# Performance work log

Measured on AMD Instinct MI355X. Metric: run time of the kernel, lower is better.

Reference implementation:

```python
import math
import jax, jax.numpy as jnp
import numpy as np

B, S, D, H, DH, R, V = 8, 1024, 1024, 8, 512, 36, 32002  # DH = d_model//2, HD = h*DH = 4096
HD = H * DH
LN_EPS = 1e-5


def setup_inputs() -> dict:
    key = jax.random.key(0)
    ks = jax.random.split(key, 16)

    def n(k, shp, std=0.02):
        return jax.random.normal(k, shp, jnp.float32) * std

    pre_words = jax.random.randint(ks[0], (B, S), 0, V)
    img_features = jax.random.normal(ks[1], (B, R, D), jnp.float32)
    exp_embed = n(ks[2], (V, D)).at[0].set(0.0)  # padding_idx=0
    # id2visual table: sparse nonneg rows over 36 regions; zero rows -> textual tokens
    id2vis = (jax.random.uniform(ks[3], (V, R)) < 0.05).astype(jnp.float32)
    # stacked params for 2 transformer layers; weights stored (in, out) so y = x @ W + b
    wq = n(ks[4], (2, D, HD)); bq = jnp.zeros((2, HD), jnp.float32)
    wk = n(ks[5], (2, D, HD)); bk = jnp.zeros((2, HD), jnp.float32)
    wv = n(ks[6], (2, D, HD)); bv = jnp.zeros((2, HD), jnp.float32)
    wo = n(ks[7], (2, HD, D)); bo = jnp.zeros((2, D), jnp.float32)
    w1 = n(ks[8], (2, D, D)); b1 = jnp.zeros((2, D), jnp.float32)
    w2 = n(ks[9], (2, D, D)); b2 = jnp.zeros((2, D), jnp.float32)
    ln1_g = jnp.ones((2, D), jnp.float32); ln1_b = jnp.zeros((2, D), jnp.float32)
    ln2_g = jnp.ones((2, D), jnp.float32); ln2_b = jnp.zeros((2, D), jnp.float32)
    return dict(pre_words=pre_words, img_features=img_features, exp_embed=exp_embed,
                id2vis=id2vis, wq=wq, bq=bq, wk=wk, bk=bk, wv=wv, bv=bv, wo=wo, bo=bo,
                w1=w1, b1=b1, w2=w2, b2=b2, ln1_g=ln1_g, ln1_b=ln1_b, ln2_g=ln2_g, ln2_b=ln2_b)


def _layer_norm(x, g, b):
    m = x.mean(-1, keepdims=True)
    v = ((x - m) ** 2).mean(-1, keepdims=True)
    return (x - m) / jnp.sqrt(v + LN_EPS) * g + b


def _softmax_one(x):
    # shifted-denominator softmax: exp(x - max) / (1 + sum exp(x - max))
    x = x - x.max(-1, keepdims=True)
    e = jnp.exp(x)
    return e / (1.0 + e.sum(-1, keepdims=True))


def reference(pre_words, img_features, exp_embed, id2vis, wq, bq, wk, bk, wv, bv,
              wo, bo, w1, b1, w2, b2, ln1_g, ln1_b, ln2_g, ln2_b):
    # token embedding: textual (masked to 0 where a visual row exists) + visual bmm
    te = exp_embed[pre_words]                       # (B,S,D)
    vids = id2vis[pre_words]                        # (B,S,R)
    word_mask = vids.sum(-1, keepdims=True) != 0    # (B,S,1)
    ve = jnp.einsum('bsr,brd->bsd', vids, img_features)
    x = jnp.where(word_mask, 0.0, te) + ve          # (B,S,D)

    scale = 1.0 / math.sqrt(DH)
    for i in range(2):  # two structurally identical transformer layers
        h = _layer_norm(x, ln1_g[i], ln1_b[i])
        q = (h @ wq[i] + bq[i]).reshape(B, S, H, DH).transpose(0, 2, 1, 3)
        k = (h @ wk[i] + bk[i]).reshape(B, S, H, DH).transpose(0, 2, 1, 3)
        v = (h @ wv[i] + bv[i]).reshape(B, S, H, DH).transpose(0, 2, 1, 3)
        attn = _softmax_one(jnp.einsum('bhqd,bhkd->bhqk', q, k) * scale)  # (B,H,S,S)
        o = jnp.einsum('bhqk,bhkd->bhqd', attn, v)
        o = o.transpose(0, 2, 1, 3).reshape(B, S, HD)
        x = x + (o @ wo[i] + bo[i])
        f = _layer_norm(x, ln2_g[i], ln2_b[i])
        f = jax.nn.gelu(f @ w1[i] + b1[i], approximate=False) @ w2[i] + b2[i]
        x = x + f
    return x
```

## Files before the change

### kernel.cpp

```cpp
#include <hip/hip_runtime.h>


using u16 = unsigned short;
typedef __attribute__((ext_vector_type(8))) short bf16x8;
typedef __attribute__((ext_vector_type(4))) float f32x4;

__device__ __forceinline__ float b2f(u16 u) {
  union { unsigned int i; float f; } v; v.i = ((unsigned int)u) << 16; return v.f;
}
__device__ __forceinline__ u16 f2b(float f) {
  union { float f; unsigned int i; } v; v.f = f;
  unsigned int i = v.i;
  return (u16)((i + 0x7FFFu + ((i >> 16) & 1u)) >> 16);
}
__device__ __forceinline__ float gelu_f(float x) {
  return 0.5f * x * (1.f + erff(x * 0.70710678118654752f));
}
__device__ __forceinline__ void async16(void* lds, const void* g) {
  __builtin_amdgcn_global_load_lds((const __attribute__((address_space(1))) void*)g,
                                   (__attribute__((address_space(3))) void*)lds, 16, 0, 0);
}
__device__ __forceinline__ void storeC(float* p, float v) { *p = v; }
__device__ __forceinline__ void storeC(u16* p, float v) { *p = f2b(v); }

__global__ __launch_bounds__(256) void embed_k(
    const int* __restrict__ words, const float* __restrict__ img,
    const float* __restrict__ emb, const float* __restrict__ id2v,
    float* __restrict__ x)
{
  __shared__ float vs[36];
  int tok = blockIdx.x, b = tok >> 10, t = threadIdx.x;
  int wd = words[tok];
  if (t < 36) vs[t] = id2v[(size_t)wd * 36 + t];
  __syncthreads();
  bool any = false;
#pragma unroll
  for (int r = 0; r < 36; ++r) any = any || (vs[r] != 0.f);
#pragma unroll
  for (int i = 0; i < 4; ++i) {
    int d = t + (i << 8);
    float acc = 0.f;
    for (int r = 0; r < 36; ++r) {
      float vv = vs[r];
      if (vv != 0.f) acc += vv * img[((size_t)(b * 36 + r) << 10) + d];
    }
    float te = any ? 0.f : emb[((size_t)wd << 10) + d];
    x[((size_t)tok << 10) + d] = te + acc;
  }
}

__global__ __launch_bounds__(256) void ln_k(
    const float* __restrict__ x, u16* __restrict__ out,
    const float* __restrict__ g, const float* __restrict__ bb)
{
  __shared__ float red[4];
  int row = blockIdx.x, t = threadIdx.x;
  const float4 xv = *(const float4*)(x + ((size_t)row << 10) + (t << 2));
  float s = xv.x + xv.y + xv.z + xv.w;
#pragma unroll
  for (int o = 32; o; o >>= 1) s += __shfl_xor(s, o, 64);
  if ((t & 63) == 0) red[t >> 6] = s;
  __syncthreads();
  s = red[0] + red[1] + red[2] + red[3];
  float mean = s * 0.0009765625f;
  float dx = xv.x - mean, dy = xv.y - mean, dz = xv.z - mean, dw = xv.w - mean;
  float q = dx * dx + dy * dy + dz * dz + dw * dw;
  __syncthreads();
#pragma unroll
  for (int o = 32; o; o >>= 1) q += __shfl_xor(q, o, 64);
  if ((t & 63) == 0) red[t >> 6] = q;
  __syncthreads();
  q = red[0] + red[1] + red[2] + red[3];
  float rstd = rsqrtf(q * 0.0009765625f + 1e-5f);
  const float4 gv = *(const float4*)(g + (t << 2));
  const float4 bv = *(const float4*)(bb + (t << 2));
  ushort4 o4;
  o4.x = f2b(dx * rstd * gv.x + bv.x);
  o4.y = f2b(dy * rstd * gv.y + bv.y);
  o4.z = f2b(dz * rstd * gv.z + bv.z);
  o4.w = f2b(dw * rstd * gv.w + bv.w);
  *(ushort4*)(out + ((size_t)row << 10) + (t << 2)) = o4;
}

__global__ __launch_bounds__(256) void sm_k(const u16* __restrict__ S, u16* __restrict__ P)
{
  size_t row = ((size_t)blockIdx.x << 2) + (threadIdx.x >> 6);
  const int lane = threadIdx.x & 63;
  const u16* sr = S + (row << 10) + (lane << 4);
  ushort4 sv[4];
#pragma unroll
  for (int i = 0; i < 4; ++i) sv[i] = *(const ushort4*)(sr + (i << 2));
  float v[16];
#pragma unroll
  for (int i = 0; i < 4; ++i) {
    v[4 * i + 0] = b2f(sv[i].x); v[4 * i + 1] = b2f(sv[i].y);
    v[4 * i + 2] = b2f(sv[i].z); v[4 * i + 3] = b2f(sv[i].w);
  }
  float m = v[0];
#pragma unroll
  for (int i = 1; i < 16; ++i) m = fmaxf(m, v[i]);
#pragma unroll
  for (int o = 32; o; o >>= 1) m = fmaxf(m, __shfl_xor(m, o, 64));
  float s = 0.f;
#pragma unroll
  for (int i = 0; i < 16; ++i) { v[i] = __expf(v[i] - m); s += v[i]; }
#pragma unroll
  for (int o = 32; o; o >>= 1) s += __shfl_xor(s, o, 64);
  const float inv = 1.f / (1.f + s);
  u16* pr = P + (row << 10) + (lane << 4);
#pragma unroll
  for (int i = 0; i < 4; ++i) {
    ushort4 pv;
    pv.x = f2b(v[4 * i + 0] * inv); pv.y = f2b(v[4 * i + 1] * inv);
    pv.z = f2b(v[4 * i + 2] * inv); pv.w = f2b(v[4 * i + 3] * inv);
    *(ushort4*)(pr + (i << 2)) = pv;
  }
}

__global__ __launch_bounds__(256) void tr_k(
    const float* __restrict__ src, u16* __restrict__ dst, int ls, int ld)
{
  __shared__ u16 tile[64][65];
  int c0 = blockIdx.x << 6, r0 = blockIdx.y << 6;
  int tx = threadIdx.x & 63, ty0 = threadIdx.x >> 6;
#pragma unroll
  for (int i = 0; i < 16; ++i) {
    int ty = (ty0 << 4) + i;
    tile[ty][tx] = f2b(src[(size_t)(r0 + ty) * ls + (c0 + tx)]);
  }
  __syncthreads();
#pragma unroll
  for (int i = 0; i < 16; ++i) {
    int ty = (ty0 << 4) + i;
    dst[(size_t)(c0 + ty) * ld + (r0 + tx)] = tile[tx][ty];
  }
}

template <typename CT, int ACT, int BIAS, int RESID, int SPLIT>
__global__ __launch_bounds__(512, 1) void gemm8p(
    const u16* __restrict__ A, const u16* __restrict__ Bt,
    CT* __restrict__ C, const float* __restrict__ bias,
    const float* __restrict__ resid,
    int M, int N, int K, int lda, int ldb, int ldc, float scale,
    int zbase, int zdiv, int ga, int gb, int gc,
    long long aS1, long long aS2, long long bS1, long long bS2,
    long long cS1, long long cS2,
    const float* __restrict__ bias2, CT* __restrict__ C2)
{
  __shared__ u16 lA[2][256 * 32];
  __shared__ u16 lB[2][256 * 32];
  const int nwg = gridDim.x * gridDim.y;
  const int id = blockIdx.y * gridDim.x + blockIdx.x;
  const int qq = nwg >> 3, rr8 = nwg & 7;
  const int xcd = id & 7, off = id >> 3;
  const int swz = (xcd < rr8 ? xcd * (qq + 1) : rr8 * (qq + 1) + (xcd - rr8) * qq) + off;
  const int bx = swz % gridDim.x, by = swz / gridDim.x;

  long long lz = blockIdx.z;
  long long gz = zbase + lz;
  long long zA = ga ? gz : lz, zB = gb ? gz : lz, zC = gc ? gz : lz;
  size_t aOff = (size_t)((zA / zdiv) * aS1 + (zA % zdiv) * aS2);
  size_t bOff = (size_t)((zB / zdiv) * bS1 + (zB % zdiv) * bS2);
  size_t cOff = (size_t)((zC / zdiv) * cS1 + (zC % zdiv) * cS2);
  const int m0 = by << 8, n0 = bx << 8;
  const int tid = threadIdx.x, lane = tid & 63, w = tid >> 6;
  const int wm = w >> 2, wn = w & 3;
  const int srow = lane >> 2;
  const int schunk = (lane & 3) ^ (srow & 3);
  const int fr = lane & 15, hi = lane >> 4;
  const int so = ((hi ^ (fr & 3)) << 3);
  const int aRow = ((wm << 7) + fr) << 5;
  const int bRow = ((wn << 6) + fr) << 5;

  f32x4 acc[8][4];
#pragma unroll
  for (int mi = 0; mi < 8; ++mi)
#pragma unroll
    for (int ni = 0; ni < 4; ++ni) acc[mi][ni] = 0.f;

  const u16* Ab = A + aOff;
  const u16* Bb = Bt + bOff;

  auto ST = [&](int buf, int k0) {
#pragma unroll
    for (int i = 0; i < 2; ++i) {
      const int rb = (w << 5) + (i << 4);
      async16(&lA[buf][rb << 5], Ab + (size_t)(m0 + rb + srow) * lda + (k0 + (schunk << 3)));
      async16(&lB[buf][rb << 5], Bb + (size_t)(n0 + rb + srow) * ldb + (k0 + (schunk << 3)));
    }
  };

  const int nt = K >> 5;
  ST(0, 0);
  ST(1, 32);
  for (int t = 0; t < nt; ++t) {
    const int cur = t & 1;
    if (t + 1 < nt) asm volatile("s_waitcnt vmcnt(4)" ::: "memory");
    else            asm volatile("s_waitcnt vmcnt(0)" ::: "memory");
    __builtin_amdgcn_s_barrier();

    bf16x8 a8[8], b8[4];
#pragma unroll
    for (int mi = 0; mi < 8; ++mi)
      a8[mi] = *(const bf16x8*)&lA[cur][aRow + mi * 512 + so];
#pragma unroll
    for (int ni = 0; ni < 4; ++ni)
      b8[ni] = *(const bf16x8*)&lB[cur][bRow + ni * 512 + so];

    __builtin_amdgcn_s_setprio(1);
#pragma unroll
    for (int mi = 0; mi < 8; ++mi)
#pragma unroll
      for (int ni = 0; ni < 4; ++ni)
        acc[mi][ni] = __builtin_amdgcn_mfma_f32_16x16x32_bf16(a8[mi], b8[ni], acc[mi][ni], 0, 0, 0);
    __builtin_amdgcn_s_setprio(0);

    asm volatile("s_waitcnt lgkmcnt(0)" ::: "memory");
    __builtin_amdgcn_s_barrier();
    if (t + 2 < nt) ST(cur, (t + 2) << 5);
  }

  const int r4 = hi << 2, cc = fr;
  const int half = N >> 1;
#pragma unroll
  for (int mi = 0; mi < 8; ++mi) {
#pragma unroll
    for (int ni = 0; ni < 4; ++ni) {
      const int col = n0 + (wn << 6) + (ni << 4) + cc;
      CT* Cd = C;
      int colx = col;
      const float* bp = bias;
      if (SPLIT && col >= half) { Cd = C2; colx = col - half; bp = bias2; }
      float bcol = 0.f;
      if (BIAS == 1) bcol = bp[colx];
#pragma unroll
      for (int j = 0; j < 4; ++j) {
        const int row = m0 + (wm << 7) + (mi << 4) + r4 + j;
        float v = acc[mi][ni][j] * scale + bcol;
        if (BIAS == 2) v += bias[row];
        if (ACT == 1) v = gelu_f(v);
        const size_t idx = cOff + (size_t)row * ldc + colx;
        if (RESID) v += resid[idx];
        storeC(&Cd[idx], v);
      }
    }
  }
}

template <typename CT, int ACT, int BIAS, int RESID>
__global__ __launch_bounds__(512, 1) void gemm8pn(
    const u16* __restrict__ A, const u16* __restrict__ Bt,
    CT* __restrict__ C, const float* __restrict__ bias,
    const float* __restrict__ resid,
    int M, int N, int K, int lda, int ldb, int ldc, float scale)
{
  __shared__ u16 lA[2][128 * 64];
  __shared__ u16 lB[2][256 * 64];
  const int nwg = gridDim.x * gridDim.y;
  const int id = blockIdx.y * gridDim.x + blockIdx.x;
  const int qq = nwg >> 3, rr8 = nwg & 7;
  const int xcd = id & 7, off = id >> 3;
  const int swz = (xcd < rr8 ? xcd * (qq + 1) : rr8 * (qq + 1) + (xcd - rr8) * qq) + off;
  const int bx = swz % gridDim.x, by = swz / gridDim.x;

  const int m0 = by << 7, n0 = bx << 8;
  const int tid = threadIdx.x, lane = tid & 63, w = tid >> 6;
  const int wm = w >> 2, wn = w & 3;
  const int srow8 = lane >> 3;
  const int schunk = (lane & 7) ^ srow8;
  const int fr = lane & 15, hi = lane >> 4;
  const int so0 = ((hi ^ (fr & 7)) << 3);
  const int so1 = (((4 + hi) ^ (fr & 7)) << 3);
  const int aRow = ((wm << 6) + fr) << 6;
  const int bRow = ((wn << 6) + fr) << 6;

  f32x4 acc[4][4];
#pragma unroll
  for (int mi = 0; mi < 4; ++mi)
#pragma unroll
    for (int ni = 0; ni < 4; ++ni) acc[mi][ni] = 0.f;

  auto ST = [&](int buf, int k0) {
#pragma unroll
    for (int s = 0; s < 2; ++s) {
      const int rb = (s << 6) + (w << 3);
      async16(&lA[buf][rb << 6], A + (size_t)(m0 + rb + srow8) * lda + (k0 + (schunk << 3)));
    }
#pragma unroll
    for (int s = 0; s < 4; ++s) {
      const int rb = (s << 6) + (w << 3);
      async16(&lB[buf][rb << 6], Bt + (size_t)(n0 + rb + srow8) * ldb + (k0 + (schunk << 3)));
    }
  };

  const int nt = K >> 6;
  ST(0, 0);
  ST(1, 64);
  for (int t = 0; t < nt; ++t) {
    const int cur = t & 1;
    if (t + 1 < nt) asm volatile("s_waitcnt vmcnt(6)" ::: "memory");
    else            asm volatile("s_waitcnt vmcnt(0)" ::: "memory");
    __builtin_amdgcn_s_barrier();

    const u16* bA0 = &lA[cur][aRow + so0];
    const u16* bA1 = &lA[cur][aRow + so1];
    const u16* bB0 = &lB[cur][bRow + so0];
    const u16* bB1 = &lB[cur][bRow + so1];

    bf16x8 a8[4][2], b8[4][2];
#pragma unroll
    for (int mi = 0; mi < 4; ++mi) {
      a8[mi][0] = *(const bf16x8*)(bA0 + mi * 1024);
      a8[mi][1] = *(const bf16x8*)(bA1 + mi * 1024);
    }
#pragma unroll
    for (int ni = 0; ni < 4; ++ni) {
      b8[ni][0] = *(const bf16x8*)(bB0 + ni * 1024);
      b8[ni][1] = *(const bf16x8*)(bB1 + ni * 1024);
    }
    __builtin_amdgcn_s_setprio(1);
#pragma unroll
    for (int mi = 0; mi < 4; ++mi)
#pragma unroll
      for (int ni = 0; ni < 4; ++ni)
#pragma unroll
        for (int ks = 0; ks < 2; ++ks)
          acc[mi][ni] = __builtin_amdgcn_mfma_f32_16x16x32_bf16(a8[mi][ks], b8[ni][ks],
                                                               acc[mi][ni], 0, 0, 0);
    __builtin_amdgcn_s_setprio(0);
    asm volatile("s_waitcnt lgkmcnt(0)" ::: "memory");
    if (t + 2 < nt) {
      __builtin_amdgcn_s_barrier();
      ST(cur, (t + 2) << 6);
    }
  }

  const int r4 = hi << 2, cc = fr;
#pragma unroll
  for (int mi = 0; mi < 4; ++mi) {
#pragma unroll
    for (int ni = 0; ni < 4; ++ni) {
      const int col = n0 + (wn << 6) + (ni << 4) + cc;
      float bcol = 0.f;
      if (BIAS == 1) bcol = bias[col];
#pragma unroll
      for (int j = 0; j < 4; ++j) {
        const int row = m0 + (wm << 6) + (mi << 4) + r4 + j;
        float v = acc[mi][ni][j] * scale + bcol;
        if (ACT == 1) v = gelu_f(v);
        const size_t idx = (size_t)row * ldc + col;
        if (RESID) v += resid[idx];
        storeC(&C[idx], v);
      }
    }
  }
}

extern "C" void kernel_launch(void* const* d_in, const int* in_sizes, int n_in,
                              void* d_out, int out_size, void* d_ws, size_t ws_size,
                              hipStream_t stream)
{
  (void)in_sizes; (void)n_in; (void)out_size;
  const int*   pre_words = (const int*)d_in[0];
  const float* img  = (const float*)d_in[1];
  const float* emb  = (const float*)d_in[2];
  const float* id2v = (const float*)d_in[3];
  const float* wq = (const float*)d_in[4];  const float* bq = (const float*)d_in[5];
  const float* wk = (const float*)d_in[6];  const float* bk = (const float*)d_in[7];
  const float* wv = (const float*)d_in[8];  const float* bv = (const float*)d_in[9];
  const float* wo = (const float*)d_in[10]; const float* bo = (const float*)d_in[11];
  const float* w1 = (const float*)d_in[12]; const float* b1 = (const float*)d_in[13];
  const float* w2 = (const float*)d_in[14]; const float* b2 = (const float*)d_in[15];
  const float* ln1g = (const float*)d_in[16]; const float* ln1b = (const float*)d_in[17];
  const float* ln2g = (const float*)d_in[18]; const float* ln2b = (const float*)d_in[19];

  const size_t FIXED = 88080384 + (size_t)(1 << 16);
  int g = 1;
  for (int c = 8; c >= 1; c >>= 1)
    if (FIXED + (size_t)c * 25165824 + 2097152 <= ws_size) { g = c; break; }
  int nc = 1;
  int ncmax = 8 * g > 64 ? 64 : 8 * g;
  for (int c = ncmax; c >= 1; c >>= 1)
    if (FIXED + (size_t)g * 25165824 + (size_t)c * 2097152 <= ws_size) { nc = c; break; }

  char* p = (char*)d_ws;
  auto alloc = [&](size_t bytes) -> void* {
    void* r = (void*)p; p += (bytes + 255) & ~(size_t)255; return r;
  };
  float* x  = (float*)alloc((size_t)8192 * 1024 * 4);
  u16* h    = (u16*)alloc((size_t)8192 * 1024 * 2);
  u16* Qg   = (u16*)alloc((size_t)g * 1024 * 4096 * 2);
  u16* Og   = Qg;
  u16* ff   = Qg;
  u16* Kg   = (u16*)alloc((size_t)g * 1024 * 4096 * 2);
  u16* Vtg  = (u16*)alloc((size_t)g * 4096 * 1024 * 2);
  u16* wqkt = (u16*)alloc((size_t)8192 * 1024 * 2);
  u16* wvt  = (u16*)alloc((size_t)4096 * 1024 * 2);
  u16* wot  = (u16*)alloc((size_t)1024 * 4096 * 2);
  u16* w1t  = (u16*)alloc((size_t)1024 * 1024 * 2);
  u16* w2t  = (u16*)alloc((size_t)1024 * 1024 * 2);
  u16* Sc   = (u16*)alloc((size_t)nc << 21);

  embed_k<<<8192, 256, 0, stream>>>(pre_words, img, emb, id2v, x);

  const float qk_scale = 0.044194173824159216f;
  for (int L = 0; L < 2; ++L) {
    const float* WQ = wq + (size_t)L * 1024 * 4096;
    const float* WK = wk + (size_t)L * 1024 * 4096;
    const float* WV = wv + (size_t)L * 1024 * 4096;
    const float* WO = wo + (size_t)L * 4096 * 1024;
    const float* W1 = w1 + (size_t)L * 1024 * 1024;
    const float* W2 = w2 + (size_t)L * 1024 * 1024;

    tr_k<<<dim3(64, 16), 256, 0, stream>>>(WQ, wqkt, 4096, 1024);
    tr_k<<<dim3(64, 16), 256, 0, stream>>>(WK, wqkt + (size_t)4096 * 1024, 4096, 1024);
    tr_k<<<dim3(64, 16), 256, 0, stream>>>(WV, wvt, 4096, 1024);
    tr_k<<<dim3(16, 64), 256, 0, stream>>>(WO, wot, 1024, 4096);
    tr_k<<<dim3(16, 16), 256, 0, stream>>>(W1, w1t, 1024, 1024);
    tr_k<<<dim3(16, 16), 256, 0, stream>>>(W2, w2t, 1024, 1024);

    ln_k<<<8192, 256, 0, stream>>>(x, h, ln1g + L * 1024, ln1b + L * 1024);

    for (int g0 = 0; g0 < 8; g0 += g) {
      const u16* hg = h + (size_t)g0 * 1048576;
      const int Mg = 1024 * g;
      gemm8p<u16, 0, 1, 0, 1><<<dim3(32, Mg >> 8), 512, 0, stream>>>(
          hg, wqkt, Qg, bq + (size_t)L * 4096, nullptr,
          Mg, 8192, 1024, 1024, 1024, 4096, 1.f,
          0, 1, 0, 0, 0, 0, 0, 0, 0, 0, 0,
          bk + (size_t)L * 4096, Kg);
      gemm8p<u16, 0, 2, 0, 0><<<dim3(4, 16, g), 512, 0, stream>>>(
          wvt, h, Vtg, bv + (size_t)L * 4096, nullptr,
          4096, 1024, 1024, 1024, 1024, 1024, 1.f,
          g0, 1, 0, 1, 0, 0, 0, 1048576LL, 0, 4194304LL, 0,
          nullptr, nullptr);
      for (int c0 = 0; c0 < 8 * g; c0 += nc) {
        gemm8p<u16, 0, 0, 0, 0><<<dim3(4, 4, nc), 512, 0, stream>>>(
            Qg, Kg, Sc, nullptr, nullptr,
            1024, 1024, 512, 4096, 4096, 1024, qk_scale,
            c0, 8, 1, 1, 0,
            4194304LL, 512LL, 4194304LL, 512LL, 8388608LL, 1048576LL,
            nullptr, nullptr);
        sm_k<<<nc << 8, 256, 0, stream>>>(Sc, Sc);
        gemm8p<u16, 0, 0, 0, 0><<<dim3(2, 4, nc), 512, 0, stream>>>(
            Sc, Vtg, Og, nullptr, nullptr,
            1024, 512, 1024, 1024, 1024, 4096, 1.f,
            c0, 8, 0, 1, 1,
            8388608LL, 1048576LL, 4194304LL, 524288LL, 4194304LL, 512LL,
            nullptr, nullptr);
      }
      gemm8pn<float, 0, 1, 1><<<dim3(4, Mg >> 7), 512, 0, stream>>>(
          Og, wot, x + (size_t)g0 * 1048576, bo + (size_t)L * 1024,
          x + (size_t)g0 * 1048576,
          Mg, 1024, 4096, 4096, 4096, 1024, 1.f);
    }

    ln_k<<<8192, 256, 0, stream>>>(x, h, ln2g + L * 1024, ln2b + L * 1024);

    gemm8pn<u16, 1, 1, 0><<<dim3(4, 64), 512, 0, stream>>>(
        h, w1t, ff, b1 + (size_t)L * 1024, nullptr,
        8192, 1024, 1024, 1024, 1024, 1024, 1.f);
    float* cdst = (L == 1) ? (float*)d_out : x;
    gemm8pn<float, 0, 1, 1><<<dim3(4, 64), 512, 0, stream>>>(
        ff, w2t, cdst, b2 + (size_t)L * 1024, x,
        8192, 1024, 1024, 1024, 1024, 1024, 1.f);
  }
}
```

Before: 1.620 ms.

## Restructure 256x256 GEMM to 4 waves with 128x128 warp tiles and BK=64

The main gemm8p kernel drops from 8 waves to 4 per workgroup. Each wave now computes a 128x128 sub-tile (8x8 MFMA accumulators), and the K step doubles to 64, which also doubles LDS buffers to 64 KB. LDS fragment loads are split into two halves with a partial lgkmcnt wait, so the first MFMA batch can start while the second half loads. The goal is higher register-level reuse and fewer barriers per K, at the cost of much higher VGPR pressure (256 accumulator floats per lane) and less latency hiding from fewer waves. The second GEMM kernel also moves its lgkmcnt wait before the MFMAs.

```diff
diff --git a/kernel.cpp b/kernel.cpp
--- a/kernel.cpp
+++ b/kernel.cpp
@@ -137,7 +137,7 @@
 }
 
 template <typename CT, int ACT, int BIAS, int RESID, int SPLIT>
-__global__ __launch_bounds__(512, 1) void gemm8p(
+__global__ __launch_bounds__(256, 1) void gemm8p(
     const u16* __restrict__ A, const u16* __restrict__ Bt,
     CT* __restrict__ C, const float* __restrict__ bias,
     const float* __restrict__ resid,
@@ -147,8 +147,8 @@
     long long cS1, long long cS2,
     const float* __restrict__ bias2, CT* __restrict__ C2)
 {
-  __shared__ u16 lA[2][256 * 32];
-  __shared__ u16 lB[2][256 * 32];
+  __shared__ u16 lA[2][256 * 64];
+  __shared__ u16 lB[2][256 * 64];
   const int nwg = gridDim.x * gridDim.y;
   const int id = blockIdx.y * gridDim.x + blockIdx.x;
   const int qq = nwg >> 3, rr8 = nwg & 7;
@@ -164,60 +164,81 @@
   size_t cOff = (size_t)((zC / zdiv) * cS1 + (zC % zdiv) * cS2);
   const int m0 = by << 8, n0 = bx << 8;
   const int tid = threadIdx.x, lane = tid & 63, w = tid >> 6;
-  const int wm = w >> 2, wn = w & 3;
-  const int srow = lane >> 2;
-  const int schunk = (lane & 3) ^ (srow & 3);
+  const int wm = w >> 1, wn = w & 1;
+  const int srow8 = lane >> 3;
+  const int schunk = (lane & 7) ^ srow8;
   const int fr = lane & 15, hi = lane >> 4;
-  const int so = ((hi ^ (fr & 3)) << 3);
-  const int aRow = ((wm << 7) + fr) << 5;
-  const int bRow = ((wn << 6) + fr) << 5;
-
-  f32x4 acc[8][4];
+  const int so0 = ((hi ^ (fr & 7)) << 3);
+  const int so1 = (((4 + hi) ^ (fr & 7)) << 3);
+  const int aRow = ((wm << 7) + fr) << 6;
+  const int bRow = ((wn << 7) + fr) << 6;
+
+  f32x4 acc[8][8];
 #pragma unroll
   for (int mi = 0; mi < 8; ++mi)
 #pragma unroll
-    for (int ni = 0; ni < 4; ++ni) acc[mi][ni] = 0.f;
+    for (int ni = 0; ni < 8; ++ni) acc[mi][ni] = 0.f;
 
   const u16* Ab = A + aOff;
   const u16* Bb = Bt + bOff;
 
   auto ST = [&](int buf, int k0) {
 #pragma unroll
-    for (int i = 0; i < 2; ++i) {
-      const int rb = (w << 5) + (i << 4);
-      async16(&lA[buf][rb << 5], Ab + (size_t)(m0 + rb + srow) * lda + (k0 + (schunk << 3)));
-      async16(&lB[buf][rb << 5], Bb + (size_t)(n0 + rb + srow) * ldb + (k0 + (schunk << 3)));
+    for (int i = 0; i < 8; ++i) {
+      const int rb = (w << 6) + (i << 3);
+      async16(&lA[buf][rb << 6], Ab + (size_t)(m0 + rb + srow8) * lda + (k0 + (schunk << 3)));
+      async16(&lB[buf][rb << 6], Bb + (size_t)(n0 + rb + srow8) * ldb + (k0 + (schunk << 3)));
     }
   };
 
-  const int nt = K >> 5;
+  const int nt = K >> 6;
   ST(0, 0);
-  ST(1, 32);
+  ST(1, 64);
   for (int t = 0; t < nt; ++t) {
     const int cur = t & 1;
-    if (t + 1 < nt) asm volatile("s_waitcnt vmcnt(4)" ::: "memory");
+    if (t + 1 < nt) asm volatile("s_waitcnt vmcnt(16)" ::: "memory");
     else            asm volatile("s_waitcnt vmcnt(0)" ::: "memory");
     __builtin_amdgcn_s_barrier();
-
-    bf16x8 a8[8], b8[4];
+    __builtin_amdgcn_sched_barrier(0);
+
+    const u16* bA0 = &lA[cur][aRow + so0];
+    const u16* bA1 = &lA[cur][aRow + so1];
+    const u16* bB0 = &lB[cur][bRow + so0];
+    const u16* bB1 = &lB[cur][bRow + so1];
+
+    bf16x8 a0[8], b0[8];
+#pragma unroll
+    for (int mi = 0; mi < 8; ++mi) a0[mi] = *(const bf16x8*)(bA0 + mi * 1024);
+#pragma unroll
+    for (int ni = 0; ni < 8; ++ni) b0[ni] = *(const bf16x8*)(bB0 + ni * 1024);
+    __builtin_amdgcn_sched_barrier(0);
+    bf16x8 a1[8], b1[8];
+#pragma unroll
+    for (int mi = 0; mi < 8; ++mi) a1[mi] = *(const bf16x8*)(bA1 + mi * 1024);
+#pragma unroll
+    for (int ni = 0; ni < 8; ++ni) b1[ni] = *(const bf16x8*)(bB1 + ni * 1024);
+
+    asm volatile("s_waitcnt lgkmcnt(15)" ::: "memory");
+    __builtin_amdgcn_sched_barrier(0);
+    __builtin_amdgcn_s_setprio(1);
 #pragma unroll
     for (int mi = 0; mi < 8; ++mi)
-      a8[mi] = *(const bf16x8*)&lA[cur][aRow + mi * 512 + so];
-#pragma unroll
-    for (int ni = 0; ni < 4; ++ni)
-      b8[ni] = *(const bf16x8*)&lB[cur][bRow + ni * 512 + so];
-
+#pragma unroll
+      for (int ni = 0; ni < 8; ++ni)
+        acc[mi][ni] = __builtin_amdgcn_mfma_f32_16x16x32_bf16(a0[mi], b0[ni], acc[mi][ni], 0, 0, 0);
+    __builtin_amdgcn_s_setprio(0);
+    asm volatile("s_waitcnt lgkmcnt(0)" ::: "memory");
+    __builtin_amdgcn_sched_barrier(0);
     __builtin_amdgcn_s_setprio(1);
 #pragma unroll
     for (int mi = 0; mi < 8; ++mi)
 #pragma unroll
-      for (int ni = 0; ni < 4; ++ni)
-        acc[mi][ni] = __builtin_amdgcn_mfma_f32_16x16x32_bf16(a8[mi], b8[ni], acc[mi][ni], 0, 0, 0);
+      for (int ni = 0; ni < 8; ++ni)
+        acc[mi][ni] = __builtin_amdgcn_mfma_f32_16x16x32_bf16(a1[mi], b1[ni], acc[mi][ni], 0, 0, 0);
     __builtin_amdgcn_s_setprio(0);
 
-    asm volatile("s_waitcnt lgkmcnt(0)" ::: "memory");
     __builtin_amdgcn_s_barrier();
-    if (t + 2 < nt) ST(cur, (t + 2) << 5);
+    if (t + 2 < nt) ST(cur, (t + 2) << 6);
   }
 
   const int r4 = hi << 2, cc = fr;
@@ -225,8 +246,8 @@
 #pragma unroll
   for (int mi = 0; mi < 8; ++mi) {
 #pragma unroll
-    for (int ni = 0; ni < 4; ++ni) {
-      const int col = n0 + (wn << 6) + (ni << 4) + cc;
+    for (int ni = 0; ni < 8; ++ni) {
+      const int col = n0 + (wn << 7) + (ni << 4) + cc;
       CT* Cd = C;
       int colx = col;
       const float* bp = bias;
@@ -318,6 +339,8 @@
       b8[ni][0] = *(const bf16x8*)(bB0 + ni * 1024);
       b8[ni][1] = *(const bf16x8*)(bB1 + ni * 1024);
     }
+    asm volatile("s_waitcnt lgkmcnt(0)" ::: "memory");
+    __builtin_amdgcn_sched_barrier(0);
     __builtin_amdgcn_s_setprio(1);
 #pragma unroll
     for (int mi = 0; mi < 4; ++mi)
@@ -328,7 +351,6 @@
           acc[mi][ni] = __builtin_amdgcn_mfma_f32_16x16x32_bf16(a8[mi][ks], b8[ni][ks],
                                                                acc[mi][ni], 0, 0, 0);
     __builtin_amdgcn_s_setprio(0);
-    asm volatile("s_waitcnt lgkmcnt(0)" ::: "memory");
     if (t + 2 < nt) {
       __builtin_amdgcn_s_barrier();
       ST(cur, (t + 2) << 6);
@@ -424,25 +446,25 @@
     for (int g0 = 0; g0 < 8; g0 += g) {
       const u16* hg = h + (size_t)g0 * 1048576;
       const int Mg = 1024 * g;
-      gemm8p<u16, 0, 1, 0, 1><<<dim3(32, Mg >> 8), 512, 0, stream>>>(
+      gemm8p<u16, 0, 1, 0, 1><<<dim3(32, Mg >> 8), 256, 0, stream>>>(
           hg, wqkt, Qg, bq + (size_t)L * 4096, nullptr,
           Mg, 8192, 1024, 1024, 1024, 4096, 1.f,
           0, 1, 0, 0, 0, 0, 0, 0, 0, 0, 0,
           bk + (size_t)L * 4096, Kg);
-      gemm8p<u16, 0, 2, 0, 0><<<dim3(4, 16, g), 512, 0, stream>>>(
+      gemm8p<u16, 0, 2, 0, 0><<<dim3(4, 16, g), 256, 0, stream>>>(
           wvt, h, Vtg, bv + (size_t)L * 4096, nullptr,
           4096, 1024, 1024, 1024, 1024, 1024, 1.f,
           g0, 1, 0, 1, 0, 0, 0, 1048576LL, 0, 4194304LL, 0,
           nullptr, nullptr);
       for (int c0 = 0; c0 < 8 * g; c0 += nc) {
-        gemm8p<u16, 0, 0, 0, 0><<<dim3(4, 4, nc), 512, 0, stream>>>(
+        gemm8p<u16, 0, 0, 0, 0><<<dim3(4, 4, nc), 256, 0, stream>>>(
             Qg, Kg, Sc, nullptr, nullptr,
             1024, 1024, 512, 4096, 4096, 1024, qk_scale,
             c0, 8, 1, 1, 0,
             4194304LL, 512LL, 4194304LL, 512LL, 8388608LL, 1048576LL,
             nullptr, nullptr);
         sm_k<<<nc << 8, 256, 0, stream>>>(Sc, Sc);
-        gemm8p<u16, 0, 0, 0, 0><<<dim3(2, 4, nc), 512, 0, stream>>>(
+        gemm8p<u16, 0, 0, 0, 0><<<dim3(2, 4, nc), 256, 0, stream>>>(
             Sc, Vtg, Og, nullptr, nullptr,
             1024, 512, 1024, 1024, 1024, 4096, 1.f,
             c0, 8, 0, 1, 1,
```

Measured after the change: 1.618 ms. Within noise of the previous version (-0.1%).
